# Optimization experiments

Hardware: AMD Instinct MI355X
Metric: run time of the kernel (lower is better)

Reference implementation:

```python
import jax, jax.numpy as jnp
import numpy as np

T, S, N, E, H, FF = 1024, 2048, 4, 1024, 16, 4096
HD = E // H
EPS = 1e-5


def layer_norm(x, g, b):
    mu = jnp.mean(x, axis=-1, keepdims=True)
    var = jnp.mean(jnp.square(x - mu), axis=-1, keepdims=True)
    return (x - mu) / jnp.sqrt(var + EPS) * g + b


def mha(q_in, k_in, v_in, w_in, b_in, w_out, b_out):
    # q_in: (T,N,E), k_in/v_in: (S,N,E); matches torch F.linear with (3E,E) weight
    t, n, e = q_in.shape
    s = k_in.shape[0]
    wq, wk, wv = jnp.split(w_in, 3, axis=0)
    bq, bk, bv = jnp.split(b_in, 3)
    q = (q_in @ wq.T + bq) * (HD ** -0.5)
    k = k_in @ wk.T + bk
    v = v_in @ wv.T + bv
    # (L,N,E) -> (N*H, L, HD)
    q = q.reshape(t, n * H, HD).transpose(1, 0, 2)
    k = k.reshape(s, n * H, HD).transpose(1, 0, 2)
    v = v.reshape(s, n * H, HD).transpose(1, 0, 2)
    attn = jax.nn.softmax(jnp.einsum('bth,bsh->bts', q, k), axis=-1)
    out = jnp.einsum('bts,bsh->bth', attn, v)  # (N*H, T, HD)
    out = out.transpose(1, 0, 2).reshape(t, n, e)
    return out @ w_out.T + b_out


def setup_inputs() -> dict:
    key = jax.random.key(0)
    ks = jax.random.split(key, 16)
    p = lambda k, shape: jax.random.normal(k, shape, dtype=jnp.float32) * 0.02
    return {
        'tgt': jax.random.normal(ks[0], (T, N, E), dtype=jnp.float32),
        'memory': jax.random.normal(ks[1], (S, N, E), dtype=jnp.float32),
        'sa_w_in': p(ks[2], (3 * E, E)), 'sa_b_in': jnp.zeros((3 * E,), jnp.float32),
        'sa_w_out': p(ks[3], (E, E)), 'sa_b_out': jnp.zeros((E,), jnp.float32),
        'ca_w_in': p(ks[4], (3 * E, E)), 'ca_b_in': jnp.zeros((3 * E,), jnp.float32),
        'ca_w_out': p(ks[5], (E, E)), 'ca_b_out': jnp.zeros((E,), jnp.float32),
        'w1': p(ks[6], (FF, E)), 'b1': jnp.zeros((FF,), jnp.float32),
        'w2': p(ks[7], (E, FF)), 'b2': jnp.zeros((E,), jnp.float32),
        'ln1_g': jnp.ones((E,), jnp.float32), 'ln1_b': jnp.zeros((E,), jnp.float32),
        'ln2_g': jnp.ones((E,), jnp.float32), 'ln2_b': jnp.zeros((E,), jnp.float32),
        'ln3_g': jnp.ones((E,), jnp.float32), 'ln3_b': jnp.zeros((E,), jnp.float32),
    }


def reference(tgt, memory, sa_w_in, sa_b_in, sa_w_out, sa_b_out,
              ca_w_in, ca_b_in, ca_w_out, ca_b_out,
              w1, b1, w2, b2, ln1_g, ln1_b, ln2_g, ln2_b, ln3_g, ln3_b):
    # self-attention block (post-LN residual); dropout = identity (eval mode)
    tgt2 = mha(tgt, tgt, tgt, sa_w_in, sa_b_in, sa_w_out, sa_b_out)
    x = layer_norm(tgt + tgt2, ln1_g, ln1_b)
    # cross-attention block
    tgt2 = mha(x, memory, memory, ca_w_in, ca_b_in, ca_w_out, ca_b_out)
    x = layer_norm(x + tgt2, ln2_g, ln2_b)
    # FFN with relu
    tgt2 = jax.nn.relu(x @ w1.T + b1) @ w2.T + b2
    return layer_norm(x + tgt2, ln3_g, ln3_b)
```

## Files before the change

### kernel.cpp

```cpp
#include <hip/hip_runtime.h>


typedef __bf16 bf16x8 __attribute__((ext_vector_type(8)));
typedef float  f32x4  __attribute__((ext_vector_type(4)));
typedef float  f32x16 __attribute__((ext_vector_type(16)));

#define T_  1024
#define S_  2048
#define NB_ 4
#define E_  1024
#define H_  16
#define HD_ 64
#define FF_ 4096
#define M1_ (T_*NB_)
#define M2_ (S_*NB_)
#define LOG2E 1.44269504088896f

__device__ __forceinline__ unsigned short f2bf(float f){
  unsigned int u = __builtin_bit_cast(unsigned int, f);
  u += 0x7fffu + ((u>>16)&1u);
  return (unsigned short)(u>>16);
}
__device__ __forceinline__ float bf2f(unsigned short h){
  unsigned int u = ((unsigned int)h)<<16;
  return __builtin_bit_cast(float, u);
}

__device__ __forceinline__ void gload16(unsigned short* l, const unsigned short* g){
  __builtin_amdgcn_global_load_lds(
      (const __attribute__((address_space(1))) unsigned int*)g,
      (__attribute__((address_space(3))) unsigned int*)l, 16, 0, 0);
}

__device__ __forceinline__ void perm32swap(unsigned &a, unsigned &b){
  asm("v_permlane32_swap_b32 %0, %1" : "+v"(a), "+v"(b));
}

struct CvtSeg { const float* s; unsigned short* d; int n4; };
struct CvtArgs { CvtSeg seg[8]; int blk_end[8]; };
__global__ __launch_bounds__(256) void f2b_multi_k(CvtArgs a){
  const int b = blockIdx.x;
  int si = 0;
  #pragma unroll
  for (int i=0;i<8;i++) if (b >= a.blk_end[i]) si = i+1;
  const int base = si ? a.blk_end[si-1] : 0;
  const int i4 = (b - base)*256 + threadIdx.x;
  if (i4 >= a.seg[si].n4) return;
  float4 f = ((const float4*)a.seg[si].s)[i4];
  union { unsigned short u[4]; uint2 v; } t;
  t.u[0]=f2bf(f.x); t.u[1]=f2bf(f.y); t.u[2]=f2bf(f.z); t.u[3]=f2bf(f.w);
  ((uint2*)a.seg[si].d)[i4] = t.v;
}

template<int FLAGS, int BN>
__global__ __launch_bounds__(256) void gemm_k(
    const unsigned short* __restrict__ A, int lda,
    const unsigned short* __restrict__ B, int ldb,
    const float* __restrict__ bias,
    const float* __restrict__ res,
    unsigned short* __restrict__ Cb, float* __restrict__ Cf,
    int M, int N, int K)
{
  constexpr int NW = BN/32;
  __shared__ unsigned short a_sh[128*64];
  __shared__ unsigned short b_sh[BN*64];
  const int tid  = threadIdx.x;
  const int wave = tid>>6;
  const int lane = tid&63;
  const int l15 = lane&15, l4 = lane>>4;
  const int row0 = blockIdx.x*128, col0 = blockIdx.y*BN;
  const int wm = (wave>>1)*64, wn = (wave&1)*(BN/2);

  const int lrow = tid>>3;
  const int scol = ((tid&7) ^ (lrow&7)) << 3;
  const int dst8 = (tid&7) << 3;

  f32x4 acc[4][NW] = {};

  for (int k0=0; k0<K; k0+=64){
    const unsigned short* ga = A + (size_t)(row0+lrow)*lda + k0 + scol;
    const unsigned short* gb = B + (size_t)(col0+lrow)*ldb + k0 + scol;
    #pragma unroll
    for (int i=0;i<4;i++)
      gload16(&a_sh[(lrow + i*32)*64 + dst8], ga + (size_t)(i*32)*lda);
    #pragma unroll
    for (int i=0;i<BN/32;i++)
      gload16(&b_sh[(lrow + i*32)*64 + dst8], gb + (size_t)(i*32)*ldb);
    __syncthreads();
    #pragma unroll
    for (int kk=0;kk<2;kk++){
      const int sw = (((kk<<2)|l4) ^ (l15&7)) << 3;
      bf16x8 af[4], bfr[NW];
      #pragma unroll
      for (int m=0;m<4;m++)  af[m]  = *(const bf16x8*)&a_sh[(wm + m*16 + l15)*64 + sw];
      #pragma unroll
      for (int n=0;n<NW;n++) bfr[n] = *(const bf16x8*)&b_sh[(wn + n*16 + l15)*64 + sw];
      #pragma unroll
      for (int m=0;m<4;m++)
        #pragma unroll
        for (int n=0;n<NW;n++)
          acc[m][n] = __builtin_amdgcn_mfma_f32_16x16x32_bf16(af[m], bfr[n], acc[m][n], 0,0,0);
    }
    __syncthreads();
  }

  #pragma unroll
  for (int m=0;m<4;m++){
    #pragma unroll
    for (int r=0;r<4;r++){
      const int rr = row0 + wm + m*16 + l4*4 + r;
      #pragma unroll
      for (int n=0;n<NW;n++){
        const int cc = col0 + wn + n*16 + l15;
        float v = acc[m][n][r] + bias[cc];
        if (FLAGS & 1) v = fmaxf(v, 0.f);
        if (FLAGS & 2) v += res[(size_t)rr*N + cc];
        if (FLAGS & 4) Cb[(size_t)rr*N + cc] = f2bf(v);
        if (FLAGS & 8) Cf[(size_t)rr*N + cc] = v;
      }
    }
  }
}

template<int BN>
__global__ __launch_bounds__(256) void gemm_splitk_k(
    const unsigned short* __restrict__ A, int lda,
    const unsigned short* __restrict__ B, int ldb,
    const float* __restrict__ bias,
    const float* __restrict__ res,
    float* __restrict__ P0, float* __restrict__ P1,
    int M, int N, int K)
{
  constexpr int NW = BN/32;
  __shared__ unsigned short a_sh[128*64];
  __shared__ unsigned short b_sh[BN*64];
  const int tid  = threadIdx.x;
  const int wave = tid>>6;
  const int lane = tid&63;
  const int l15 = lane&15, l4 = lane>>4;
  const int row0 = blockIdx.x*128, col0 = blockIdx.y*BN;
  const int wm = (wave>>1)*64, wn = (wave&1)*(BN/2);
  const int z = blockIdx.z;
  const int kh = K>>1;
  const int kbeg = z*kh;

  const int lrow = tid>>3;
  const int scol = ((tid&7) ^ (lrow&7)) << 3;
  const int dst8 = (tid&7) << 3;

  f32x4 acc[4][NW] = {};

  for (int k0=kbeg; k0<kbeg+kh; k0+=64){
    const unsigned short* ga = A + (size_t)(row0+lrow)*lda + k0 + scol;
    const unsigned short* gb = B + (size_t)(col0+lrow)*ldb + k0 + scol;
    #pragma unroll
    for (int i=0;i<4;i++)
      gload16(&a_sh[(lrow + i*32)*64 + dst8], ga + (size_t)(i*32)*lda);
    #pragma unroll
    for (int i=0;i<BN/32;i++)
      gload16(&b_sh[(lrow + i*32)*64 + dst8], gb + (size_t)(i*32)*ldb);
    __syncthreads();
    #pragma unroll
    for (int kk=0;kk<2;kk++){
      const int sw = (((kk<<2)|l4) ^ (l15&7)) << 3;
      bf16x8 af[4], bfr[NW];
      #pragma unroll
      for (int m=0;m<4;m++)  af[m]  = *(const bf16x8*)&a_sh[(wm + m*16 + l15)*64 + sw];
      #pragma unroll
      for (int n=0;n<NW;n++) bfr[n] = *(const bf16x8*)&b_sh[(wn + n*16 + l15)*64 + sw];
      #pragma unroll
      for (int m=0;m<4;m++)
        #pragma unroll
        for (int n=0;n<NW;n++)
          acc[m][n] = __builtin_amdgcn_mfma_f32_16x16x32_bf16(af[m], bfr[n], acc[m][n], 0,0,0);
    }
    __syncthreads();
  }

  float* out = z ? P1 : P0;
  #pragma unroll
  for (int m=0;m<4;m++){
    #pragma unroll
    for (int r=0;r<4;r++){
      const int rr = row0 + wm + m*16 + l4*4 + r;
      #pragma unroll
      for (int n=0;n<NW;n++){
        const int cc = col0 + wn + n*16 + l15;
        float v = acc[m][n][r];
        if (!z) v += bias[cc] + res[(size_t)rr*N + cc];
        out[(size_t)rr*N + cc] = v;
      }
    }
  }
}

template<int BN>
__global__ __launch_bounds__(256) void gemm_scat_k(
    const unsigned short* __restrict__ A, int lda,
    const unsigned short* __restrict__ B, int ldb,
    const float* __restrict__ bias,
    unsigned short* __restrict__ qb, unsigned short* __restrict__ kb,
    unsigned short* __restrict__ vtb,
    int M, int N, int K, int nq, int nk, int Lq, int Lkv, float qscale)
{
  constexpr int NW = BN/32;
  constexpr int SMEM_ELEMS = (BN==128) ? (128*132) : (128*64 + BN*64);
  __shared__ unsigned short smem[SMEM_ELEMS];
  unsigned short* a_sh = smem;
  unsigned short* b_sh = smem + 128*64;
  const int tid  = threadIdx.x;
  const int wave = tid>>6, lane = tid&63;
  const int l15 = lane&15, l4 = lane>>4;
  const int row0 = blockIdx.x*128, col0 = blockIdx.y*BN;
  const int wm = (wave>>1)*64, wn = (wave&1)*(BN/2);

  const int lrow = tid>>3;
  const int scol = ((tid&7) ^ (lrow&7)) << 3;
  const int dst8 = (tid&7) << 3;

  f32x4 acc[4][NW] = {};

  for (int k0=0; k0<K; k0+=64){
    const unsigned short* ga = A + (size_t)(row0+lrow)*lda + k0 + scol;
    const unsigned short* gb = B + (size_t)(col0+lrow)*ldb + k0 + scol;
    #pragma unroll
    for (int i=0;i<4;i++)
      gload16(&a_sh[(lrow + i*32)*64 + dst8], ga + (size_t)(i*32)*lda);
    #pragma unroll
    for (int i=0;i<BN/32;i++)
      gload16(&b_sh[(lrow + i*32)*64 + dst8], gb + (size_t)(i*32)*ldb);
    __syncthreads();
    #pragma unroll
    for (int kk=0;kk<2;kk++){
      const int sw = (((kk<<2)|l4) ^ (l15&7)) << 3;
      bf16x8 af[4], bfr[NW];
      #pragma unroll
      for (int m=0;m<4;m++)  af[m]  = *(const bf16x8*)&a_sh[(wm + m*16 + l15)*64 + sw];
      #pragma unroll
      for (int n=0;n<NW;n++) bfr[n] = *(const bf16x8*)&b_sh[(wn + n*16 + l15)*64 + sw];
      #pragma unroll
      for (int m=0;m<4;m++)
        #pragma unroll
        for (int n=0;n<NW;n++)
          acc[m][n] = __builtin_amdgcn_mfma_f32_16x16x32_bf16(af[m], bfr[n], acc[m][n], 0,0,0);
    }
    __syncthreads();
  }

  if (col0 < nq + nk){
    const bool isq = (col0 < nq);
    unsigned short* dst = isq ? qb : kb;
    const int  base  = isq ? 0 : nq;
    const int  L     = isq ? Lq : Lkv;
    const float scale = isq ? qscale : 1.0f;
    #pragma unroll
    for (int m=0;m<4;m++){
      #pragma unroll
      for (int r=0;r<4;r++){
        const int rr = row0 + wm + m*16 + l4*4 + r;
        const int t = rr>>2, nn = rr&3;
        #pragma unroll
        for (int n=0;n<NW;n++){
          const int cc = col0 + wn + n*16 + l15;
          const int e = cc - base, h = e>>6, d = e&63;
          const float v = (acc[m][n][r] + bias[cc]) * scale;
          dst[((size_t)(nn*H_ + h)*L + t)*HD_ + d] = f2bf(v);
        }
      }
    }
  } else if constexpr (BN == 128){
    unsigned short* cT = smem;
    #pragma unroll
    for (int m=0;m<4;m++){
      const int tl = ((wm + m*16)>>2) + l4;
      #pragma unroll
      for (int n=0;n<4;n++){
        const int ccl = wn + n*16 + l15;
        const float bi = bias[col0 + ccl];
        #pragma unroll
        for (int r=0;r<4;r++)
          cT[ccl*132 + r*32 + tl] = f2bf(acc[m][n][r] + bi);
      }
    }
    __syncthreads();
    const int t0 = row0>>2;
    const int tl4 = tid&7, c5 = tid>>3;
    const int voff = nq + nk;
    #pragma unroll
    for (int i=0;i<16;i++){
      const int combo = i*32 + c5;
      const int nn = combo&3, ccl = combo>>2;
      const int e = col0 + ccl - voff, h = e>>6, d = e&63;
      const uint2 val = *(const uint2*)&cT[ccl*132 + nn*32 + tl4*4];
      *(uint2*)(vtb + (size_t)((nn*H_ + h)*HD_ + d)*Lkv + t0 + tl4*4) = val;
    }
  }
}

template<bool PARTIAL>
__global__ __launch_bounds__(256) void attn_k(
    const unsigned short* __restrict__ qb, const unsigned short* __restrict__ kb,
    const unsigned short* __restrict__ vtb,
    unsigned short* __restrict__ o_out, float* __restrict__ l_out,
    int T, int S, int s_count)
{
  __shared__ unsigned short k_sh[2][64*64];
  __shared__ unsigned short v_sh[2][64*64];
  __shared__ float bc_sh[4][32];
  const int tid  = threadIdx.x;
  const int wave = tid>>6, lane = tid&63;
  const int l31  = lane&31;
  const int hv   = lane>>5;
  const int bh   = blockIdx.x;
  const int z    = blockIdx.z;
  const int s_begin = z * s_count;
  const int q0   = blockIdx.y*128 + wave*32;
  const size_t qbase = (size_t)bh*T*HD_;
  const size_t kbase = (size_t)bh*S*HD_;
  const size_t vbase = (size_t)bh*HD_*S;

  const int strow = tid>>3;
  const int stch  = tid&7;
  const int sc_sw = (stch ^ (strow&7)) << 3;
  const int dst8  = stch<<3;

  {
    const unsigned short* gk = kb  + kbase + (size_t)s_begin*HD_;
    const unsigned short* gv = vtb + vbase + s_begin;
    #pragma unroll
    for (int i=0;i<2;i++){
      const int row = strow + 32*i;
      gload16(&k_sh[0][row*64 + dst8], gk + (size_t)row*HD_ + sc_sw);
      gload16(&v_sh[0][row*64 + dst8], gv + (size_t)row*S   + sc_sw);
    }
  }

  bf16x8 qf[4];
  #pragma unroll
  for (int p=0;p<4;p++)
    qf[p] = *(const bf16x8*)(qb + qbase + (size_t)(q0 + l31)*HD_ + p*16 + hv*8);

  f32x16 o0 = {}, o1 = {};
  float l_run = 0.f;

  int cur = 0;
  for (int s0=s_begin; s0<s_begin+s_count; s0+=64){
    if (s0 + 64 < s_begin + s_count){
      const int nxt = cur^1;
      const unsigned short* gk = kb  + kbase + (size_t)(s0+64)*HD_;
      const unsigned short* gv = vtb + vbase + (s0+64);
      #pragma unroll
      for (int i=0;i<2;i++){
        const int row = strow + 32*i;
        gload16(&k_sh[nxt][row*64 + dst8], gk + (size_t)row*HD_ + sc_sw);
        gload16(&v_sh[nxt][row*64 + dst8], gv + (size_t)row*S   + sc_sw);
      }
      asm volatile("s_waitcnt vmcnt(4)" ::: "memory");
    } else {
      asm volatile("s_waitcnt vmcnt(0)" ::: "memory");
    }
    __builtin_amdgcn_s_barrier();

    const unsigned short* ksh = k_sh[cur];
    const unsigned short* vsh = v_sh[cur];

    f32x16 sc0 = {}, sc1 = {};
    __builtin_amdgcn_s_setprio(1);
    #pragma unroll
    for (int p=0;p<4;p++){
      const int slot = 2*p + hv;
      bf16x8 kf0 = *(const bf16x8*)&ksh[(l31     )*64 + ((slot ^ (l31&7))<<3)];
      bf16x8 kf1 = *(const bf16x8*)&ksh[(l31 + 32)*64 + ((slot ^ (l31&7))<<3)];
      sc0 = __builtin_amdgcn_mfma_f32_32x32x16_bf16(kf0, qf[p], sc0, 0,0,0);
      sc1 = __builtin_amdgcn_mfma_f32_32x32x16_bf16(kf1, qf[p], sc1, 0,0,0);
    }
    __builtin_amdgcn_s_setprio(0);

    float rs = 0.f;
    #pragma unroll
    for (int r=0;r<16;r++){
      sc0[r] = __builtin_amdgcn_exp2f(sc0[r]);
      sc1[r] = __builtin_amdgcn_exp2f(sc1[r]);
      rs += sc0[r] + sc1[r];
    }
    {
      unsigned ra = __builtin_bit_cast(unsigned, rs), rb = ra;
      perm32swap(ra, rb);
      l_run += rs + __builtin_bit_cast(float, hv ? ra : rb);
    }

    bf16x8 pa[4];
    #pragma unroll
    for (int ks=0;ks<4;ks++){
      const int base = 8*(ks&1);
      unsigned pkA0, pkA1, pkB0, pkB1;
      if (ks < 2){
        asm("v_cvt_pk_bf16_f32 %0, %1, %2" : "=v"(pkA0) : "v"(sc0[base+0]), "v"(sc0[base+1]));
        asm("v_cvt_pk_bf16_f32 %0, %1, %2" : "=v"(pkA1) : "v"(sc0[base+2]), "v"(sc0[base+3]));
        asm("v_cvt_pk_bf16_f32 %0, %1, %2" : "=v"(pkB0) : "v"(sc0[base+4]), "v"(sc0[base+5]));
        asm("v_cvt_pk_bf16_f32 %0, %1, %2" : "=v"(pkB1) : "v"(sc0[base+6]), "v"(sc0[base+7]));
      } else {
        asm("v_cvt_pk_bf16_f32 %0, %1, %2" : "=v"(pkA0) : "v"(sc1[base+0]), "v"(sc1[base+1]));
        asm("v_cvt_pk_bf16_f32 %0, %1, %2" : "=v"(pkA1) : "v"(sc1[base+2]), "v"(sc1[base+3]));
        asm("v_cvt_pk_bf16_f32 %0, %1, %2" : "=v"(pkB0) : "v"(sc1[base+4]), "v"(sc1[base+5]));
        asm("v_cvt_pk_bf16_f32 %0, %1, %2" : "=v"(pkB1) : "v"(sc1[base+6]), "v"(sc1[base+7]));
      }
      perm32swap(pkA0, pkB0);
      perm32swap(pkA1, pkB1);
      union { unsigned w[4]; bf16x8 v; } u;
      u.w[0] = pkA0; u.w[1] = pkA1; u.w[2] = pkB0; u.w[3] = pkB1;
      pa[ks] = u.v;
    }

    __builtin_amdgcn_s_setprio(1);
    #pragma unroll
    for (int ks=0;ks<4;ks++){
      const int slot = 2*ks + hv;
      bf16x8 vf0 = *(const bf16x8*)&vsh[(l31     )*64 + ((slot ^ (l31&7))<<3)];
      bf16x8 vf1 = *(const bf16x8*)&vsh[(l31 + 32)*64 + ((slot ^ (l31&7))<<3)];
      o0 = __builtin_amdgcn_mfma_f32_32x32x16_bf16(pa[ks], vf0, o0, 0,0,0);
      o1 = __builtin_amdgcn_mfma_f32_32x32x16_bf16(pa[ks], vf1, o1, 0,0,0);
    }
    __builtin_amdgcn_s_setprio(0);

    __builtin_amdgcn_s_barrier();
    cur ^= 1;
  }

  if constexpr (PARTIAL){
    const size_t obase = (size_t)(z*64 + bh)*T;
    #pragma unroll
    for (int r=0;r<16;r++){
      const int qr = (r&3) + 8*(r>>2) + 4*hv;
      unsigned short* op = o_out + (obase + q0 + qr)*HD_;
      op[l31]      = f2bf(o0[r]);
      op[l31 + 32] = f2bf(o1[r]);
    }
    if (hv == 0) l_out[obase + q0 + l31] = l_run;
  } else {
    bc_sh[wave][l31] = 1.f / l_run;
    const int nb = bh>>4, hh = bh&15;
    #pragma unroll
    for (int r=0;r<16;r++){
      const int qr  = (r&3) + 8*(r>>2) + 4*hv;
      const float inv = bc_sh[wave][qr];
      const int t = q0 + qr;
      unsigned short* op = o_out + ((size_t)t*NB_ + nb)*E_ + hh*HD_;
      op[l31]      = f2bf(o0[r]*inv);
      op[l31 + 32] = f2bf(o1[r]*inv);
    }
  }
}

__global__ __launch_bounds__(256) void comb_k(
    const unsigned short* __restrict__ opart, const float* __restrict__ lpart,
    unsigned short* __restrict__ outb, int T)
{
  const int bh = blockIdx.y;
  const int t  = blockIdx.x*4 + (threadIdx.x>>6);
  const int d  = threadIdx.x&63;
  const size_t half = (size_t)64*T;
  const size_t row  = (size_t)bh*T + t;
  const float o = bf2f(opart[row*HD_ + d]) + bf2f(opart[(half + row)*HD_ + d]);
  const float l = lpart[row] + lpart[half + row];
  const int nb = bh>>4, hh = bh&15;
  outb[((size_t)t*NB_ + nb)*E_ + hh*HD_ + d] = f2bf(o / l);
}

__global__ __launch_bounds__(256) void ln_k(
    const float* __restrict__ p0, const float* __restrict__ p1,
    const float* __restrict__ g, const float* __restrict__ bb,
    float* __restrict__ of, unsigned short* __restrict__ ob)
{
  const int row = blockIdx.x, tid = threadIdx.x;
  const size_t base = (size_t)row*E_;
  float v[4];
  #pragma unroll
  for (int i=0;i<4;i++){
    const int col = tid + 256*i;
    v[i] = p0[base + col] + p1[base + col];
  }
  float s  = v[0]+v[1]+v[2]+v[3];
  float s2 = v[0]*v[0]+v[1]*v[1]+v[2]*v[2]+v[3]*v[3];
  #pragma unroll
  for (int off=32; off>0; off>>=1){
    s  += __shfl_down(s, off);
    s2 += __shfl_down(s2, off);
  }
  __shared__ float red[8];
  if ((tid&63)==0){ red[tid>>6] = s; red[4+(tid>>6)] = s2; }
  __syncthreads();
  s  = red[0]+red[1]+red[2]+red[3];
  s2 = red[4]+red[5]+red[6]+red[7];
  const float mu   = s * (1.f/E_);
  const float var  = s2 * (1.f/E_) - mu*mu;
  const float rstd = rsqrtf(var + 1e-5f);
  #pragma unroll
  for (int i=0;i<4;i++){
    const int col = tid + 256*i;
    const float y = (v[i]-mu)*rstd*g[col] + bb[col];
    if (of) of[base + col] = y;
    if (ob) ob[base + col] = f2bf(y);
  }
}

extern "C" void kernel_launch(void* const* d_in, const int* in_sizes, int n_in,
                              void* d_out, int out_size, void* d_ws, size_t ws_size,
                              hipStream_t stream)
{
  const float* tgt      = (const float*)d_in[0];
  const float* mem      = (const float*)d_in[1];
  const float* sa_w_in  = (const float*)d_in[2];
  const float* sa_b_in  = (const float*)d_in[3];
  const float* sa_w_out = (const float*)d_in[4];
  const float* sa_b_out = (const float*)d_in[5];
  const float* ca_w_in  = (const float*)d_in[6];
  const float* ca_b_in  = (const float*)d_in[7];
  const float* ca_w_out = (const float*)d_in[8];
  const float* ca_b_out = (const float*)d_in[9];
  const float* w1 = (const float*)d_in[10];
  const float* b1 = (const float*)d_in[11];
  const float* w2 = (const float*)d_in[12];
  const float* b2 = (const float*)d_in[13];
  const float* ln1_g=(const float*)d_in[14]; const float* ln1_b=(const float*)d_in[15];
  const float* ln2_g=(const float*)d_in[16]; const float* ln2_b=(const float*)d_in[17];
  const float* ln3_g=(const float*)d_in[18]; const float* ln3_b=(const float*)d_in[19];

  char* ws = (char*)d_ws;
  size_t off = 0;
  auto alloc = [&](size_t bytes)->char* {
    char* p = ws + off; off += (bytes + 255) & ~(size_t)255; return p;
  };
  unsigned short* w_sa_in_b  = (unsigned short*)alloc((size_t)3*E_*E_*2);
  unsigned short* w_sa_out_b = (unsigned short*)alloc((size_t)E_*E_*2);
  unsigned short* w_ca_in_b  = (unsigned short*)alloc((size_t)3*E_*E_*2);
  unsigned short* w_ca_out_b = (unsigned short*)alloc((size_t)E_*E_*2);
  unsigned short* w1_b  = (unsigned short*)alloc((size_t)FF_*E_*2);
  unsigned short* w2_b  = (unsigned short*)alloc((size_t)E_*FF_*2);
  unsigned short* tgt_b = (unsigned short*)alloc((size_t)M1_*E_*2);
  unsigned short* mem_b = (unsigned short*)alloc((size_t)M2_*E_*2);
  unsigned short* qbuf  = (unsigned short*)alloc((size_t)64*T_*HD_*2);
  unsigned short* kbuf  = (unsigned short*)alloc((size_t)64*S_*HD_*2);
  unsigned short* vtbuf = (unsigned short*)alloc((size_t)64*S_*HD_*2);
  unsigned short* cbuf  = (unsigned short*)alloc((size_t)M1_*FF_*2);
  unsigned short* atto  = (unsigned short*)alloc((size_t)M1_*E_*2);
  unsigned short* opart = (unsigned short*)alloc((size_t)2*64*T_*HD_*2);
  float*          lpart = (float*)alloc((size_t)2*64*T_*4);
  float* resf = (float*)alloc((size_t)M1_*E_*4);
  float* xf   = (float*)alloc((size_t)M1_*E_*4);
  unsigned short* xb = (unsigned short*)alloc((size_t)M1_*E_*2);
  (void)ws_size; (void)in_sizes; (void)n_in; (void)out_size;

  float* P1 = (float*)opart;

  const float QSCALE = 0.125f * LOG2E;

  {
    CvtArgs a;
    const float* srcs[8] = {tgt, mem, sa_w_in, sa_w_out, ca_w_in, ca_w_out, w1, w2};
    unsigned short* dsts[8] = {tgt_b, mem_b, w_sa_in_b, w_sa_out_b, w_ca_in_b, w_ca_out_b, w1_b, w2_b};
    size_t ns[8] = {(size_t)M1_*E_, (size_t)M2_*E_, (size_t)3*E_*E_, (size_t)E_*E_,
                    (size_t)3*E_*E_, (size_t)E_*E_, (size_t)FF_*E_, (size_t)E_*FF_};
    int blk = 0;
    for (int i=0;i<8;i++){
      a.seg[i].s = srcs[i]; a.seg[i].d = dsts[i]; a.seg[i].n4 = (int)(ns[i]/4);
      blk += (a.seg[i].n4 + 255)/256;
      a.blk_end[i] = blk;
    }
    f2b_multi_k<<<blk, 256, 0, stream>>>(a);
  }

  gemm_scat_k<128><<<dim3(M1_/128, (3*E_)/128), 256, 0, stream>>>(
      tgt_b, E_, w_sa_in_b, E_, sa_b_in, qbuf, kbuf, vtbuf,
      M1_, 3*E_, E_, E_, E_, T_, T_, QSCALE);
  attn_k<false><<<dim3(64, T_/128, 1), 256, 0, stream>>>(
      qbuf, kbuf, vtbuf, atto, nullptr, T_, T_, T_);
  gemm_splitk_k<64><<<dim3(M1_/128, E_/64, 2), 256, 0, stream>>>(
      atto, E_, w_sa_out_b, E_, sa_b_out, tgt, resf, P1, M1_, E_, E_);
  ln_k<<<M1_, 256, 0, stream>>>(resf, P1, ln1_g, ln1_b, xf, xb);

  gemm_scat_k<128><<<dim3(M2_/128, (2*E_)/128), 256, 0, stream>>>(
      mem_b, E_, w_ca_in_b + (size_t)E_*E_, E_, ca_b_in + E_, nullptr, kbuf, vtbuf,
      M2_, 2*E_, E_, 0, E_, T_, S_, QSCALE);
  gemm_scat_k<64><<<dim3(M1_/128, E_/64), 256, 0, stream>>>(
      xb, E_, w_ca_in_b, E_, ca_b_in, qbuf, nullptr, nullptr,
      M1_, E_, E_, E_, 0, T_, S_, QSCALE);
  attn_k<true><<<dim3(64, T_/128, 2), 256, 0, stream>>>(
      qbuf, kbuf, vtbuf, opart, lpart, T_, S_, S_/2);
  comb_k<<<dim3(T_/4, 64), 256, 0, stream>>>(opart, lpart, atto, T_);
  gemm_splitk_k<64><<<dim3(M1_/128, E_/64, 2), 256, 0, stream>>>(
      atto, E_, w_ca_out_b, E_, ca_b_out, xf, resf, P1, M1_, E_, E_);
  ln_k<<<M1_, 256, 0, stream>>>(resf, P1, ln2_g, ln2_b, xf, xb);

  gemm_k<5,128><<<dim3(M1_/128, FF_/128), 256, 0, stream>>>(
      xb, E_, w1_b, E_, b1, nullptr, cbuf, nullptr, M1_, FF_, E_);
  gemm_splitk_k<64><<<dim3(M1_/128, E_/64, 2), 256, 0, stream>>>(
      cbuf, FF_, w2_b, FF_, b2, xf, resf, P1, M1_, E_, FF_);
  ln_k<<<M1_, 256, 0, stream>>>(resf, P1, ln3_g, ln3_b, (float*)d_out, nullptr);
}
```

Baseline: 406.0 us.

## Software-pipeline attention: overlap QK^T of next tile with PV of previous

Restructures the attention kernel into a software pipeline. Each iteration issues the QK^T MFMAs for tile i together with the PV MFMAs for tile i-1, so the exp/convert softmax work of one tile can overlap with matrix-core work. K and V are now staged separately at offset tiles, the tile count becomes a compile-time template parameter with a fully unrolled loop, and launch bounds request 3 blocks per CU. This costs more registers, since two sets of P fragments are kept live, and any spill risk grows under the tighter occupancy bound.

```diff
diff --git a/kernel.cpp b/kernel.cpp
--- a/kernel.cpp
+++ b/kernel.cpp
@@ -297,13 +297,14 @@
   }
 }
 
-template<bool PARTIAL>
-__global__ __launch_bounds__(256) void attn_k(
+template<bool PARTIAL, int NT>
+__global__ __launch_bounds__(256,3) void attn_k(
     const unsigned short* __restrict__ qb, const unsigned short* __restrict__ kb,
     const unsigned short* __restrict__ vtb,
     unsigned short* __restrict__ o_out, float* __restrict__ l_out,
-    int T, int S, int s_count)
+    int T, int S)
 {
+  static_assert((NT & 1) == 0 && NT >= 4, "NT even");
   __shared__ unsigned short k_sh[2][64*64];
   __shared__ unsigned short v_sh[2][64*64];
   __shared__ float bc_sh[4][32];
@@ -313,7 +314,7 @@
   const int hv   = lane>>5;
   const int bh   = blockIdx.x;
   const int z    = blockIdx.z;
-  const int s_begin = z * s_count;
+  const int s_begin = z * (NT*64);
   const int q0   = blockIdx.y*128 + wave*32;
   const size_t qbase = (size_t)bh*T*HD_;
   const size_t kbase = (size_t)bh*S*HD_;
@@ -323,87 +324,77 @@
   const int stch  = tid&7;
   const int sc_sw = (stch ^ (strow&7)) << 3;
   const int dst8  = stch<<3;
-
-  {
-    const unsigned short* gk = kb  + kbase + (size_t)s_begin*HD_;
-    const unsigned short* gv = vtb + vbase + s_begin;
-    #pragma unroll
-    for (int i=0;i<2;i++){
-      const int row = strow + 32*i;
-      gload16(&k_sh[0][row*64 + dst8], gk + (size_t)row*HD_ + sc_sw);
-      gload16(&v_sh[0][row*64 + dst8], gv + (size_t)row*S   + sc_sw);
-    }
-  }
+  const unsigned short* gk0 = kb  + kbase + (size_t)s_begin*HD_;
+  const unsigned short* gv0 = vtb + vbase + s_begin;
+
+  auto stageK = [&](int t, int slot){
+    const unsigned short* g = gk0 + (size_t)(t*64)*HD_;
+    gload16(&k_sh[slot][(strow   )*64 + dst8], g + (size_t)(strow   )*HD_ + sc_sw);
+    gload16(&k_sh[slot][(strow+32)*64 + dst8], g + (size_t)(strow+32)*HD_ + sc_sw);
+  };
+  auto stageV = [&](int t, int slot){
+    const unsigned short* g = gv0 + t*64;
+    gload16(&v_sh[slot][(strow   )*64 + dst8], g + (size_t)(strow   )*S + sc_sw);
+    gload16(&v_sh[slot][(strow+32)*64 + dst8], g + (size_t)(strow+32)*S + sc_sw);
+  };
 
   bf16x8 qf[4];
   #pragma unroll
   for (int p=0;p<4;p++)
     qf[p] = *(const bf16x8*)(qb + qbase + (size_t)(q0 + l31)*HD_ + p*16 + hv*8);
+  asm volatile("" ::: "memory");
+
+  stageK(0, 0);
 
   f32x16 o0 = {}, o1 = {};
-  float l_run = 0.f;
-
-  int cur = 0;
-  for (int s0=s_begin; s0<s_begin+s_count; s0+=64){
-    if (s0 + 64 < s_begin + s_count){
-      const int nxt = cur^1;
-      const unsigned short* gk = kb  + kbase + (size_t)(s0+64)*HD_;
-      const unsigned short* gv = vtb + vbase + (s0+64);
-      #pragma unroll
-      for (int i=0;i<2;i++){
-        const int row = strow + 32*i;
-        gload16(&k_sh[nxt][row*64 + dst8], gk + (size_t)row*HD_ + sc_sw);
-        gload16(&v_sh[nxt][row*64 + dst8], gv + (size_t)row*S   + sc_sw);
-      }
-      asm volatile("s_waitcnt vmcnt(4)" ::: "memory");
-    } else {
-      asm volatile("s_waitcnt vmcnt(0)" ::: "memory");
-    }
-    __builtin_amdgcn_s_barrier();
-
-    const unsigned short* ksh = k_sh[cur];
-    const unsigned short* vsh = v_sh[cur];
-
-    f32x16 sc0 = {}, sc1 = {};
-    __builtin_amdgcn_s_setprio(1);
+  float rsa = 0.f, rsb = 0.f;
+  bf16x8 paA[4], paB[4];
+
+  auto QK = [&](const unsigned short* ksh, f32x16& s0, f32x16& s1){
     #pragma unroll
     for (int p=0;p<4;p++){
       const int slot = 2*p + hv;
       bf16x8 kf0 = *(const bf16x8*)&ksh[(l31     )*64 + ((slot ^ (l31&7))<<3)];
       bf16x8 kf1 = *(const bf16x8*)&ksh[(l31 + 32)*64 + ((slot ^ (l31&7))<<3)];
-      sc0 = __builtin_amdgcn_mfma_f32_32x32x16_bf16(kf0, qf[p], sc0, 0,0,0);
-      sc1 = __builtin_amdgcn_mfma_f32_32x32x16_bf16(kf1, qf[p], sc1, 0,0,0);
-    }
-    __builtin_amdgcn_s_setprio(0);
-
-    float rs = 0.f;
+      s0 = __builtin_amdgcn_mfma_f32_32x32x16_bf16(kf0, qf[p], s0, 0,0,0);
+      s1 = __builtin_amdgcn_mfma_f32_32x32x16_bf16(kf1, qf[p], s1, 0,0,0);
+    }
+  };
+  auto PV = [&](const unsigned short* vsh, const bf16x8* pa){
+    #pragma unroll
+    for (int ks=0;ks<4;ks++){
+      const int slot = 2*ks + hv;
+      bf16x8 vf0 = *(const bf16x8*)&vsh[(l31     )*64 + ((slot ^ (l31&7))<<3)];
+      bf16x8 vf1 = *(const bf16x8*)&vsh[(l31 + 32)*64 + ((slot ^ (l31&7))<<3)];
+      o0 = __builtin_amdgcn_mfma_f32_32x32x16_bf16(pa[ks], vf0, o0, 0,0,0);
+      o1 = __builtin_amdgcn_mfma_f32_32x32x16_bf16(pa[ks], vf1, o1, 0,0,0);
+    }
+  };
+  auto SM = [&](f32x16& s0, f32x16& s1, bf16x8* pa){
     #pragma unroll
     for (int r=0;r<16;r++){
-      sc0[r] = __builtin_amdgcn_exp2f(sc0[r]);
-      sc1[r] = __builtin_amdgcn_exp2f(sc1[r]);
-      rs += sc0[r] + sc1[r];
-    }
-    {
-      unsigned ra = __builtin_bit_cast(unsigned, rs), rb = ra;
-      perm32swap(ra, rb);
-      l_run += rs + __builtin_bit_cast(float, hv ? ra : rb);
-    }
-
-    bf16x8 pa[4];
+      s0[r] = __builtin_amdgcn_exp2f(s0[r]);
+      s1[r] = __builtin_amdgcn_exp2f(s1[r]);
+    }
+    #pragma unroll
+    for (int r=0;r<16;r+=2){
+      rsa += s0[r]   + s1[r];
+      rsb += s0[r+1] + s1[r+1];
+    }
     #pragma unroll
     for (int ks=0;ks<4;ks++){
       const int base = 8*(ks&1);
       unsigned pkA0, pkA1, pkB0, pkB1;
       if (ks < 2){
-        asm("v_cvt_pk_bf16_f32 %0, %1, %2" : "=v"(pkA0) : "v"(sc0[base+0]), "v"(sc0[base+1]));
-        asm("v_cvt_pk_bf16_f32 %0, %1, %2" : "=v"(pkA1) : "v"(sc0[base+2]), "v"(sc0[base+3]));
-        asm("v_cvt_pk_bf16_f32 %0, %1, %2" : "=v"(pkB0) : "v"(sc0[base+4]), "v"(sc0[base+5]));
-        asm("v_cvt_pk_bf16_f32 %0, %1, %2" : "=v"(pkB1) : "v"(sc0[base+6]), "v"(sc0[base+7]));
+        asm("v_cvt_pk_bf16_f32 %0, %1, %2" : "=v"(pkA0) : "v"(s0[base+0]), "v"(s0[base+1]));
+        asm("v_cvt_pk_bf16_f32 %0, %1, %2" : "=v"(pkA1) : "v"(s0[base+2]), "v"(s0[base+3]));
+        asm("v_cvt_pk_bf16_f32 %0, %1, %2" : "=v"(pkB0) : "v"(s0[base+4]), "v"(s0[base+5]));
+        asm("v_cvt_pk_bf16_f32 %0, %1, %2" : "=v"(pkB1) : "v"(s0[base+6]), "v"(s0[base+7]));
       } else {
-        asm("v_cvt_pk_bf16_f32 %0, %1, %2" : "=v"(pkA0) : "v"(sc1[base+0]), "v"(sc1[base+1]));
-        asm("v_cvt_pk_bf16_f32 %0, %1, %2" : "=v"(pkA1) : "v"(sc1[base+2]), "v"(sc1[base+3]));
-        asm("v_cvt_pk_bf16_f32 %0, %1, %2" : "=v"(pkB0) : "v"(sc1[base+4]), "v"(sc1[base+5]));
-        asm("v_cvt_pk_bf16_f32 %0, %1, %2" : "=v"(pkB1) : "v"(sc1[base+6]), "v"(sc1[base+7]));
+        asm("v_cvt_pk_bf16_f32 %0, %1, %2" : "=v"(pkA0) : "v"(s1[base+0]), "v"(s1[base+1]));
+        asm("v_cvt_pk_bf16_f32 %0, %1, %2" : "=v"(pkA1) : "v"(s1[base+2]), "v"(s1[base+3]));
+        asm("v_cvt_pk_bf16_f32 %0, %1, %2" : "=v"(pkB0) : "v"(s1[base+4]), "v"(s1[base+5]));
+        asm("v_cvt_pk_bf16_f32 %0, %1, %2" : "=v"(pkB1) : "v"(s1[base+6]), "v"(s1[base+7]));
       }
       perm32swap(pkA0, pkB0);
       perm32swap(pkA1, pkB1);
@@ -411,20 +402,53 @@
       u.w[0] = pkA0; u.w[1] = pkA1; u.w[2] = pkB0; u.w[3] = pkB1;
       pa[ks] = u.v;
     }
-
+  };
+
+  {
+    stageK(1, 1);
+    stageV(0, 0);
+    asm volatile("s_waitcnt vmcnt(4)" ::: "memory");
+    __builtin_amdgcn_s_barrier();
+    f32x16 s0 = {}, s1 = {};
     __builtin_amdgcn_s_setprio(1);
-    #pragma unroll
-    for (int ks=0;ks<4;ks++){
-      const int slot = 2*ks + hv;
-      bf16x8 vf0 = *(const bf16x8*)&vsh[(l31     )*64 + ((slot ^ (l31&7))<<3)];
-      bf16x8 vf1 = *(const bf16x8*)&vsh[(l31 + 32)*64 + ((slot ^ (l31&7))<<3)];
-      o0 = __builtin_amdgcn_mfma_f32_32x32x16_bf16(pa[ks], vf0, o0, 0,0,0);
-      o1 = __builtin_amdgcn_mfma_f32_32x32x16_bf16(pa[ks], vf1, o1, 0,0,0);
-    }
+    QK(k_sh[0], s0, s1);
     __builtin_amdgcn_s_setprio(0);
-
+    SM(s0, s1, paA);
     __builtin_amdgcn_s_barrier();
-    cur ^= 1;
+  }
+
+  auto BODY = [&](int i, const bf16x8* paPrev, bf16x8* paCur){
+    const int kt = (i+1 < NT) ? (i+1) : (NT-1);
+    stageK(kt, (i+1)&1);
+    stageV(i, i&1);
+    asm volatile("s_waitcnt vmcnt(4)" ::: "memory");
+    __builtin_amdgcn_s_barrier();
+    f32x16 s0 = {}, s1 = {};
+    __builtin_amdgcn_s_setprio(1);
+    QK(k_sh[i&1], s0, s1);
+    PV(v_sh[(i+1)&1], paPrev);
+    __builtin_amdgcn_s_setprio(0);
+    SM(s0, s1, paCur);
+    __builtin_amdgcn_s_barrier();
+  };
+
+  for (int ii=1; ii+1<NT; ii+=2){
+    BODY(ii,   paA, paB);
+    BODY(ii+1, paB, paA);
+  }
+  BODY(NT-1, paA, paB);
+
+  asm volatile("s_waitcnt vmcnt(0)" ::: "memory");
+  __builtin_amdgcn_s_barrier();
+  __builtin_amdgcn_s_setprio(1);
+  PV(v_sh[(NT-1)&1], paB);
+  __builtin_amdgcn_s_setprio(0);
+
+  float l_run = rsa + rsb;
+  {
+    unsigned a_ = __builtin_bit_cast(unsigned, l_run), b_ = a_;
+    perm32swap(a_, b_);
+    l_run += __builtin_bit_cast(float, hv ? a_ : b_);
   }
 
   if constexpr (PARTIAL){
@@ -573,8 +597,8 @@
   gemm_scat_k<128><<<dim3(M1_/128, (3*E_)/128), 256, 0, stream>>>(
       tgt_b, E_, w_sa_in_b, E_, sa_b_in, qbuf, kbuf, vtbuf,
       M1_, 3*E_, E_, E_, E_, T_, T_, QSCALE);
-  attn_k<false><<<dim3(64, T_/128, 1), 256, 0, stream>>>(
-      qbuf, kbuf, vtbuf, atto, nullptr, T_, T_, T_);
+  attn_k<false,16><<<dim3(64, T_/128, 1), 256, 0, stream>>>(
+      qbuf, kbuf, vtbuf, atto, nullptr, T_, T_);
   gemm_splitk_k<64><<<dim3(M1_/128, E_/64, 2), 256, 0, stream>>>(
       atto, E_, w_sa_out_b, E_, sa_b_out, tgt, resf, P1, M1_, E_, E_);
   ln_k<<<M1_, 256, 0, stream>>>(resf, P1, ln1_g, ln1_b, xf, xb);
@@ -585,8 +609,8 @@
   gemm_scat_k<64><<<dim3(M1_/128, E_/64), 256, 0, stream>>>(
       xb, E_, w_ca_in_b, E_, ca_b_in, qbuf, nullptr, nullptr,
       M1_, E_, E_, E_, 0, T_, S_, QSCALE);
-  attn_k<true><<<dim3(64, T_/128, 2), 256, 0, stream>>>(
-      qbuf, kbuf, vtbuf, opart, lpart, T_, S_, S_/2);
+  attn_k<true,16><<<dim3(64, T_/128, 2), 256, 0, stream>>>(
+      qbuf, kbuf, vtbuf, opart, lpart, T_, S_);
   comb_k<<<dim3(T_/4, 64), 256, 0, stream>>>(opart, lpart, atto, T_);
   gemm_splitk_k<64><<<dim3(M1_/128, E_/64, 2), 256, 0, stream>>>(
       atto, E_, w_ca_out_b, E_, ca_b_out, xf, resf, P1, M1_, E_, E_);
```

New measurement: 390.4 us. 3.8% less time.
